# Kernel tuning notes

Hardware: AMD Instinct MI355X
Metric: run time of the kernel (lower is better)

Reference implementation:

```python
import jax, jax.numpy as jnp
import numpy as np

B, N, NT, ET = 16, 38, 9, 4
NE = N * (N - 1) // 2          # 703 edge-generation steps
R = N + NE                     # repeat_num = 741 masked subgraphs
H = D = 128                    # nhid / nout
L = 12                         # num_flow_layer
EDIM = ET - 1                  # 3 relation types used by RGCN
EPS = 1e-5
TEMP = 0.1                     # straight-through argmax temperature


def _st_dis(x, w1, b1, w2, b2):
    # MLP -> logits -> straight-through one-hot(argmax)
    h = jnp.tanh(x @ w1.T + b1)
    logits = h @ w2.T + b2
    soft = jax.nn.softmax(logits / TEMP, axis=-1)
    hard = jax.nn.one_hot(jnp.argmax(logits, axis=-1), logits.shape[-1], dtype=logits.dtype)
    return soft + jax.lax.stop_gradient(hard - soft)


def _one_hot_add(inputs, shift):
    # (inputs + shift) mod vocab in one-hot space == circular conv via FFT
    out = jnp.fft.ifft(jnp.fft.fft(inputs, axis=-1) * jnp.fft.fft(shift, axis=-1), axis=-1)
    return jnp.real(out).astype(inputs.dtype)


def _gconv(x, adj, w):
    # x: (b, n, f_in), adj: (b, e, n, n), w: (e*f_out, f_in)
    b, n, _ = x.shape
    s = (x @ w.T).reshape(b, n, EDIM, -1)            # (b, n, e, f_out)
    return jnp.einsum('beij,bjeo->bio', adj, s)      # aggregate over relations


def _rgcn(x, adj, emb_w, gc1_w, gc2_w, gc3_w):
    h = x @ emb_w.T
    h = jax.nn.relu(_gconv(h, adj, gc1_w))
    h = jax.nn.relu(_gconv(h, adj, gc2_w))
    return _gconv(h, adj, gc3_w)                     # no relu on last layer


def setup_inputs():
    key = jax.random.key(0)
    ks = jax.random.split(key, 16)
    s = 0.1
    iu, ju = np.triu_indices(N, k=1)                 # canonical edge order (703, 2)
    return {
        'x': jax.random.uniform(ks[0], (B, N, NT), dtype=jnp.float32),
        'adj': jax.random.uniform(ks[1], (B, ET, N, N), dtype=jnp.float32),
        'x_deq': jax.random.normal(ks[2], (B, N, NT), dtype=jnp.float32),
        'adj_deq': jax.random.normal(ks[3], (B, NE, ET), dtype=jnp.float32),
        'mask_node': jax.random.uniform(ks[4], (R, N)) < 0.5,
        'mask_edge': jax.random.uniform(ks[5], (R, N, N)) < 0.5,
        'index_select_edge': jnp.asarray(np.stack([iu, ju], 1), dtype=jnp.int32),
        'emb_w': jax.random.normal(ks[6], (NT, NT), jnp.float32) * s,
        'gc1_w': jax.random.normal(ks[7], (EDIM * H, NT), jnp.float32) * s,
        'gc2_w': jax.random.normal(ks[8], (EDIM * H, H), jnp.float32) * s,
        'gc3_w': jax.random.normal(ks[9], (EDIM * D, H), jnp.float32) * s,
        'bn_gamma': jnp.ones((D,), jnp.float32),
        'bn_beta': jnp.zeros((D,), jnp.float32),
        'node_w1': jax.random.normal(ks[10], (L, H, D), jnp.float32) * s,
        'node_b1': jnp.zeros((L, H), jnp.float32),
        'node_w2': jax.random.normal(ks[11], (L, NT, H), jnp.float32) * s,
        'node_b2': jnp.zeros((L, NT), jnp.float32),
        'edge_w1': jax.random.normal(ks[12], (L, H, 3 * D), jnp.float32) * s,
        'edge_b1': jnp.zeros((L, H), jnp.float32),
        'edge_w2': jax.random.normal(ks[13], (L, ET, H), jnp.float32) * s,
        'edge_b2': jnp.zeros((L, ET), jnp.float32),
    }


def reference(x, adj, x_deq, adj_deq, mask_node, mask_edge, index_select_edge,
              emb_w, gc1_w, gc2_w, gc3_w, bn_gamma, bn_beta,
              node_w1, node_b1, node_w2, node_b2,
              edge_w1, edge_b1, edge_w2, edge_b2):
    adj3 = adj[:, :EDIM]                                              # (B,3,N,N)
    xr = jnp.where(mask_node[None, :, :, None], x[:, None], 0.0)      # (B,R,N,NT)
    ar = jnp.where(mask_edge[None, :, None], adj3[:, None], 0.0)      # (B,R,3,N,N)
    xr = xr.reshape(B * R, N, NT)
    ar = ar.reshape(B * R, EDIM, N, N)
    node_emb = _rgcn(xr, ar, emb_w, gc1_w, gc2_w, gc3_w)              # (B*R,N,D)
    # BatchNorm1d over channels (training-mode batch statistics, biased var)
    m = node_emb.mean(axis=(0, 1))
    v = node_emb.var(axis=(0, 1))
    node_emb = (node_emb - m) * jax.lax.rsqrt(v + EPS) * bn_gamma + bn_beta
    node_emb = node_emb.reshape(B, R, N, D)
    graph_emb = node_emb.sum(axis=2)                                  # (B,R,D)
    graph_emb_node = graph_emb[:, :N]                                 # (B,N,D)
    graph_emb_edge = graph_emb[:, N:, None]                           # (B,NE,1,D)
    all_node_emb_edge = node_emb[:, N:]                               # (B,NE,N,D)
    idx = jnp.broadcast_to(index_select_edge[None, :, :, None].astype(jnp.int32), (B, NE, 2, D))
    sel = jnp.take_along_axis(all_node_emb_edge, idx, axis=2)         # (B,NE,2,D)
    graph_node_emb_edge = jnp.concatenate([sel, graph_emb_edge], axis=2).reshape(B, NE, 3 * D)
    xd, ad = x_deq, adj_deq
    for i in range(L):
        nt = _st_dis(graph_emb_node, node_w1[i], node_b1[i], node_w2[i], node_b2[i]).astype(x.dtype)
        xd = _one_hot_add(xd, nt)
        et = _st_dis(graph_node_emb_edge, edge_w1[i], edge_b1[i], edge_w2[i], edge_b2[i]).astype(adj.dtype)
        ad = _one_hot_add(ad, et)
    return (xd, ad)
```

## Files before the change

### kernel.cpp

```cpp
#include <hip/hip_runtime.h>

#define B_   16
#define N_   38
#define NT_  9
#define ET_  4
#define NE_  703
#define R_   741
#define L_   12
#define BR_  11856

__global__ __launch_bounds__(128) void k_sx(const float* __restrict__ x,
                                            const float* __restrict__ emb_w,
                                            const float* __restrict__ gc1_w,
                                            float* __restrict__ sx)
{
  int bn = blockIdx.x;
  int t  = threadIdx.x;
  __shared__ float xr[NT_];
  __shared__ float hx[NT_];
  if (t < NT_) xr[t] = x[bn*NT_ + t];
  __syncthreads();
  if (t < NT_) {
    float s = 0.f;
    #pragma unroll
    for (int u = 0; u < NT_; ++u) s += xr[u] * emb_w[t*NT_ + u];
    hx[t] = s;
  }
  __syncthreads();
  for (int eo = t; eo < 384; eo += 128) {
    float s = 0.f;
    #pragma unroll
    for (int u = 0; u < NT_; ++u) s += hx[u] * gc1_w[eo*NT_ + u];
    sx[bn*384 + eo] = s;
  }
}

__global__ __launch_bounds__(128) void k_wt(const float* __restrict__ gc2_w,
                                            const float* __restrict__ gc3_w,
                                            float* __restrict__ Wt)
{
  int blk   = blockIdx.x;
  int which = blk / 384;
  int rem   = blk - which*384;
  int e     = rem >> 7;
  int k     = rem & 127;
  int o     = threadIdx.x;
  const float* src = which ? gc3_w : gc2_w;
  Wt[(((which*3 + e) << 7) + k)*128 + o] = src[((e << 7) + o)*128 + k];
}

__device__ __forceinline__ void fma4(float4& d, float a, const float4& s) {
  d.x += a*s.x; d.y += a*s.y; d.z += a*s.z; d.w += a*s.w;
}

__device__ __forceinline__ void fill_A(const float* __restrict__ adj,
                                       const int* __restrict__ mask_edge,
                                       int b, int r, int e, int tid,
                                       float* __restrict__ A4_l,
                                       float* __restrict__ A1_l)
{
  for (int m = tid; m < 38*32; m += 256) {
    int j    = m >> 5;
    int slot = m & 31;
    int i    = (slot >> 2) + ((slot & 3) << 3);
    float v  = 0.f;
    if (mask_edge[(r*N_ + i)*N_ + j]) v = adj[((b*ET_ + e)*N_ + i)*N_ + j];
    A4_l[m] = v;
  }
  for (int m = tid; m < 38*8; m += 256) {
    int j = m >> 3;
    int i = (m & 7) + 32;
    float v = 0.f;
    if (i < N_ && mask_edge[(r*N_ + i)*N_ + j]) v = adj[((b*ET_ + e)*N_ + i)*N_ + j];
    A1_l[m] = v;
  }
}

__device__ __forceinline__ void eacc_m(const float* __restrict__ A4_l,
                                       const float* __restrict__ A1_l,
                                       const float* __restrict__ S_l,
                                       int p, int c,
                                       const int* __restrict__ mn,
                                       float4 d[5])
{
  #pragma unroll 2
  for (int j = 0; j < 38; ++j) {
    if (!mn[j]) continue;
    float4 s4 = *(const float4*)&S_l[(j << 7) + (c << 2)];
    float4 a4 = *(const float4*)&A4_l[(j << 5) + (p << 2)];
    float  a1 = A1_l[(j << 3) + p];
    fma4(d[0], a4.x, s4); fma4(d[1], a4.y, s4); fma4(d[2], a4.z, s4);
    fma4(d[3], a4.w, s4); fma4(d[4], a1,   s4);
  }
}

__device__ __forceinline__ void eacc_u(const float* __restrict__ A4_l,
                                       const float* __restrict__ A1_l,
                                       const float* __restrict__ S_l,
                                       int p, int c,
                                       float4 d[5])
{
  #pragma unroll 4
  for (int j = 0; j < 38; ++j) {
    float4 s4 = *(const float4*)&S_l[(j << 7) + (c << 2)];
    float4 a4 = *(const float4*)&A4_l[(j << 5) + (p << 2)];
    float  a1 = A1_l[(j << 3) + p];
    fma4(d[0], a4.x, s4); fma4(d[1], a4.y, s4); fma4(d[2], a4.z, s4);
    fma4(d[3], a4.w, s4); fma4(d[4], a1,   s4);
  }
}

__device__ __forceinline__ void gemm_fused(const float* __restrict__ H_l,
                                           const float* __restrict__ Wb,
                                           int p, int c, float4 g[3][5])
{
  #pragma unroll
  for (int e = 0; e < 3; ++e)
    #pragma unroll
    for (int q = 0; q < 5; ++q) { g[e][q].x = 0.f; g[e][q].y = 0.f; g[e][q].z = 0.f; g[e][q].w = 0.f; }
  #pragma unroll 1
  for (int k0 = 0; k0 < 128; k0 += 4) {
    float4 h0 = *(const float4*)&H_l[((p+ 0) << 7) + k0];
    float4 h1 = *(const float4*)&H_l[((p+ 8) << 7) + k0];
    float4 h2 = *(const float4*)&H_l[((p+16) << 7) + k0];
    float4 h3 = *(const float4*)&H_l[((p+24) << 7) + k0];
    float4 h4 = *(const float4*)&H_l[((p+32) << 7) + k0];
    #pragma unroll
    for (int e = 0; e < 3; ++e) {
      const float* We = &Wb[(e << 14) + (k0 << 7) + (c << 2)];
      float4 w0 = *(const float4*)&We[  0];
      float4 w1 = *(const float4*)&We[128];
      float4 w2 = *(const float4*)&We[256];
      float4 w3 = *(const float4*)&We[384];
      fma4(g[e][0], h0.x, w0); fma4(g[e][0], h0.y, w1); fma4(g[e][0], h0.z, w2); fma4(g[e][0], h0.w, w3);
      fma4(g[e][1], h1.x, w0); fma4(g[e][1], h1.y, w1); fma4(g[e][1], h1.z, w2); fma4(g[e][1], h1.w, w3);
      fma4(g[e][2], h2.x, w0); fma4(g[e][2], h2.y, w1); fma4(g[e][2], h2.z, w2); fma4(g[e][2], h2.w, w3);
      fma4(g[e][3], h3.x, w0); fma4(g[e][3], h3.y, w1); fma4(g[e][3], h3.z, w2); fma4(g[e][3], h3.w, w3);
      fma4(g[e][4], h4.x, w0); fma4(g[e][4], h4.y, w1); fma4(g[e][4], h4.z, w2); fma4(g[e][4], h4.w, w3);
    }
  }
}

__device__ __forceinline__ void relu_store(float* __restrict__ H_l, int p, int c,
                                           const float4 d[5])
{
  #pragma unroll
  for (int q = 0; q < 5; ++q) {
    float4 t;
    t.x = fmaxf(d[q].x, 0.f); t.y = fmaxf(d[q].y, 0.f);
    t.z = fmaxf(d[q].z, 0.f); t.w = fmaxf(d[q].w, 0.f);
    *(float4*)&H_l[((p + (q << 3)) << 7) + (c << 2)] = t;
  }
}

__global__ __launch_bounds__(256) void k_rgcn(
    const float* __restrict__ adj, const int* __restrict__ mask_node,
    const int* __restrict__ mask_edge, const int* __restrict__ isel,
    const float* __restrict__ sx, const float* __restrict__ Wt,
    float* __restrict__ sumE, float* __restrict__ sumSq,
    float* __restrict__ selw)
{
  const int br  = blockIdx.x;
  const int b   = br / R_;
  const int r   = br - b*R_;
  const int tid = threadIdx.x;
  const int c   = tid & 31;
  const int p   = tid >> 5;

  __shared__ __align__(16) float A4_l[38*32];
  __shared__ __align__(16) float A1_l[38*8];
  __shared__ __align__(16) float SH_l[40*128];
  __shared__ int mn_l[40];

  if (tid < 40) mn_l[tid] = (tid < 38) ? mask_node[r*N_ + tid] : 0;
  __syncthreads();

  float4 d[5];
  #pragma unroll
  for (int q = 0; q < 5; ++q) { d[q].x = d[q].y = d[q].z = d[q].w = 0.f; }

  for (int e = 0; e < 3; ++e) {
    for (int idx = tid; idx < 40*32; idx += 256) {
      int j = idx >> 5, q4 = idx & 31;
      float4 v; v.x = v.y = v.z = v.w = 0.f;
      if (j < N_ && mn_l[j]) v = *(const float4*)&sx[(b*N_ + j)*384 + (e << 7) + (q4 << 2)];
      *(float4*)&SH_l[(j << 7) + (q4 << 2)] = v;
    }
    fill_A(adj, mask_edge, b, r, e, tid, A4_l, A1_l);
    __syncthreads();
    eacc_m(A4_l, A1_l, SH_l, p, c, mn_l, d);
    __syncthreads();
  }
  relu_store(SH_l, p, c, d);
  __syncthreads();

  for (int gv = 0; gv < 2; ++gv) {
    float4 g[3][5];
    gemm_fused(SH_l, &Wt[gv*49152], p, c, g);
    #pragma unroll
    for (int q = 0; q < 5; ++q) { d[q].x = d[q].y = d[q].z = d[q].w = 0.f; }
    #pragma unroll
    for (int e = 0; e < 3; ++e) {
      __syncthreads();
      #pragma unroll
      for (int q = 0; q < 5; ++q)
        *(float4*)&SH_l[((p + (q << 3)) << 7) + (c << 2)] = g[e][q];
      fill_A(adj, mask_edge, b, r, e, tid, A4_l, A1_l);
      __syncthreads();
      eacc_u(A4_l, A1_l, SH_l, p, c, d);
    }
    if (gv == 0) {
      __syncthreads();
      relu_store(SH_l, p, c, d);
      __syncthreads();
    }
  }
  __syncthreads();

  {
    float4 sA, sB;
    sA.x = d[0].x+d[1].x+d[2].x+d[3].x+d[4].x;
    sA.y = d[0].y+d[1].y+d[2].y+d[3].y+d[4].y;
    sA.z = d[0].z+d[1].z+d[2].z+d[3].z+d[4].z;
    sA.w = d[0].w+d[1].w+d[2].w+d[3].w+d[4].w;
    sB.x = d[0].x*d[0].x+d[1].x*d[1].x+d[2].x*d[2].x+d[3].x*d[3].x+d[4].x*d[4].x;
    sB.y = d[0].y*d[0].y+d[1].y*d[1].y+d[2].y*d[2].y+d[3].y*d[3].y+d[4].y*d[4].y;
    sB.z = d[0].z*d[0].z+d[1].z*d[1].z+d[2].z*d[2].z+d[3].z*d[3].z+d[4].z*d[4].z;
    sB.w = d[0].w*d[0].w+d[1].w*d[1].w+d[2].w*d[2].w+d[3].w*d[3].w+d[4].w*d[4].w;
    *(float4*)&SH_l[( p      << 7) + (c << 2)] = sA;
    *(float4*)&SH_l[((8 + p) << 7) + (c << 2)] = sB;
  }
  __syncthreads();
  {
    int o = tid & 127, half = tid >> 7;
    float t = 0.f;
    #pragma unroll
    for (int pp = 0; pp < 8; ++pp) t += SH_l[(((half << 3) + pp) << 7) + o];
    if (half == 0) sumE [br*128 + o] = t;
    else           sumSq[br*128 + o] = t;
  }
  if (r >= N_) {
    int k  = r - N_;
    int iu = isel[2*k], ju = isel[2*k+1];
    if (p == (iu & 7)) {
      int mu = iu >> 3;
      float4 v = d[0];
      if (mu == 1) v = d[1]; else if (mu == 2) v = d[2];
      else if (mu == 3) v = d[3]; else if (mu == 4) v = d[4];
      *(float4*)&selw[(((b*NE_ + k)*2 + 0) << 7) + (c << 2)] = v;
    }
    if (p == (ju & 7)) {
      int mu = ju >> 3;
      float4 v = d[0];
      if (mu == 1) v = d[1]; else if (mu == 2) v = d[2];
      else if (mu == 3) v = d[3]; else if (mu == 4) v = d[4];
      *(float4*)&selw[(((b*NE_ + k)*2 + 1) << 7) + (c << 2)] = v;
    }
  }
}

__global__ __launch_bounds__(256) void k_bn1(const float* __restrict__ sumE,
                                             const float* __restrict__ sumSq,
                                             double* __restrict__ part)
{
  int g = blockIdx.x;
  int t = threadIdx.x;
  int o = t & 127, h = t >> 7;
  int lo = g*47;
  int hi = lo + 47; if (hi > BR_) hi = BR_;
  double a1 = 0.0, a2 = 0.0;
  for (int i = lo + h; i < hi; i += 2) {
    a1 += (double)sumE [i*128 + o];
    a2 += (double)sumSq[i*128 + o];
  }
  __shared__ double sh1[256], sh2[256];
  sh1[t] = a1; sh2[t] = a2;
  __syncthreads();
  if (h == 0) {
    part[g*128 + o]           = sh1[o] + sh1[128 + o];
    part[256*128 + g*128 + o] = sh2[o] + sh2[128 + o];
  }
}

__global__ __launch_bounds__(128) void k_bn2(const double* __restrict__ part,
                                             const float* __restrict__ gamma,
                                             const float* __restrict__ beta,
                                             float* __restrict__ bnsc,
                                             float* __restrict__ bnsh)
{
  int o = threadIdx.x;
  double s1 = 0.0, s2 = 0.0;
  for (int g = 0; g < 256; ++g) {
    s1 += part[g*128 + o];
    s2 += part[256*128 + g*128 + o];
  }
  double cnt = (double)BR_ * 38.0;
  double m   = s1 / cnt;
  double var = s2 / cnt - m*m;
  double rs  = 1.0 / sqrt(var + 1e-5);
  double sc  = (double)gamma[o] * rs;
  bnsc[o] = (float)sc;
  bnsh[o] = beta[o] - (float)(m * sc);
}

__global__ __launch_bounds__(128) void k_node(
    const float* __restrict__ sumE, const float* __restrict__ bnsc,
    const float* __restrict__ bnsh,
    const float* __restrict__ w1, const float* __restrict__ b1,
    const float* __restrict__ w2, const float* __restrict__ b2,
    const float* __restrict__ x_deq, float* __restrict__ out)
{
  int blk = blockIdx.x;
  int b   = blk / N_;
  int o   = threadIdx.x;
  __shared__ __align__(16) float xv[128];
  __shared__ __align__(16) float hb[128];
  __shared__ float lg[NT_];
  __shared__ int   P_s;
  int br = b*R_ + (blk - b*N_);
  xv[o] = sumE[br*128 + o]*bnsc[o] + 38.f*bnsh[o];
  if (o == 0) P_s = 0;
  __syncthreads();
  for (int l = 0; l < L_; ++l) {
    const float* wr = &w1[(l*128 + o)*128];
    float s = b1[l*128 + o];
    for (int k = 0; k < 128; k += 4) {
      float4 w4 = *(const float4*)&wr[k];
      s += w4.x*xv[k] + w4.y*xv[k+1] + w4.z*xv[k+2] + w4.w*xv[k+3];
    }
    hb[o] = tanhf(s);
    __syncthreads();
    if (o < NT_) {
      const float* w2r = &w2[(l*NT_ + o)*128];
      float s2 = b2[l*NT_ + o];
      for (int k = 0; k < 128; ++k) s2 += w2r[k]*hb[k];
      lg[o] = s2;
    }
    __syncthreads();
    if (o == 0) {
      int best = 0; float bv = lg[0];
      #pragma unroll
      for (int cc = 1; cc < NT_; ++cc) if (lg[cc] > bv) { bv = lg[cc]; best = cc; }
      P_s += best;
    }
    __syncthreads();
  }
  int P = P_s % NT_;
  if (o < NT_) {
    int srcc = o - P; if (srcc < 0) srcc += NT_;
    out[blk*NT_ + o] = x_deq[blk*NT_ + srcc];
  }
}

__global__ __launch_bounds__(256) void k_edge(
    const float* __restrict__ sumE, const float* __restrict__ selw,
    const float* __restrict__ bnsc, const float* __restrict__ bnsh,
    const float* __restrict__ w1, const float* __restrict__ b1,
    const float* __restrict__ w2, const float* __restrict__ b2,
    const float* __restrict__ adj_deq, float* __restrict__ out)
{
  int k = blockIdx.x;
  int t = threadIdx.x;
  int o = t & 127, g = t >> 7;
  __shared__ __align__(16) float xv[16][384];
  __shared__ __align__(16) float hb[16][132];
  __shared__ float lg[16][4];
  __shared__ int   Pf[16];

  for (int idx = t; idx < 16*128; idx += 256) {
    int b = idx >> 7, oo = idx & 127;
    float sc = bnsc[oo], sh = bnsh[oo];
    int base = ((b*NE_ + k)*2)*128;
    xv[b][oo]       = selw[base + oo]      *sc + sh;
    xv[b][128 + oo] = selw[base + 128 + oo]*sc + sh;
    xv[b][256 + oo] = sumE[(b*R_ + N_ + k)*128 + oo]*sc + 38.f*sh;
  }
  int Preg = 0;
  __syncthreads();

  for (int l = 0; l < L_; ++l) {
    float acc[8];
    #pragma unroll
    for (int bb = 0; bb < 8; ++bb) acc[bb] = b1[l*128 + o];
    const float* wr = &w1[(l*128 + o)*384];
    for (int kk = 0; kk < 384; kk += 4) {
      float4 w4 = *(const float4*)&wr[kk];
      #pragma unroll
      for (int bb = 0; bb < 8; ++bb) {
        float4 h4 = *(const float4*)&xv[g*8 + bb][kk];
        acc[bb] += w4.x*h4.x + w4.y*h4.y + w4.z*h4.z + w4.w*h4.w;
      }
    }
    #pragma unroll
    for (int bb = 0; bb < 8; ++bb) hb[g*8 + bb][o] = tanhf(acc[bb]);
    __syncthreads();
    if (t < 64) {
      int m = t >> 2, c = t & 3;
      const float* w2r = &w2[(l*ET_ + c)*128];
      float s2 = b2[l*ET_ + c];
      for (int kk = 0; kk < 128; ++kk) s2 += w2r[kk]*hb[m][kk];
      lg[m][c] = s2;
    }
    __syncthreads();
    if (t < 16) {
      int best = 0; float bv = lg[t][0];
      #pragma unroll
      for (int c = 1; c < ET_; ++c) if (lg[t][c] > bv) { bv = lg[t][c]; best = c; }
      Preg += best;
    }
    __syncthreads();
  }
  if (t < 16) Pf[t] = Preg & 3;
  __syncthreads();
  if (t < 64) {
    int m = t >> 2, c = t & 3;
    int srcc = c - Pf[m]; if (srcc < 0) srcc += ET_;
    out[(m*NE_ + k)*ET_ + c] = adj_deq[(m*NE_ + k)*ET_ + srcc];
  }
}

extern "C" void kernel_launch(void* const* d_in, const int* in_sizes, int n_in,
                              void* d_out, int out_size, void* d_ws, size_t ws_size,
                              hipStream_t stream)
{
  (void)in_sizes; (void)n_in; (void)out_size; (void)ws_size;

  const float* x         = (const float*)d_in[0];
  const float* adj       = (const float*)d_in[1];
  const float* x_deq     = (const float*)d_in[2];
  const float* adj_deq   = (const float*)d_in[3];
  const int*   mask_node = (const int*)d_in[4];
  const int*   mask_edge = (const int*)d_in[5];
  const int*   isel      = (const int*)d_in[6];
  const float* emb_w     = (const float*)d_in[7];
  const float* gc1_w     = (const float*)d_in[8];
  const float* gc2_w     = (const float*)d_in[9];
  const float* gc3_w     = (const float*)d_in[10];
  const float* bn_gamma  = (const float*)d_in[11];
  const float* bn_beta   = (const float*)d_in[12];
  const float* node_w1   = (const float*)d_in[13];
  const float* node_b1   = (const float*)d_in[14];
  const float* node_w2   = (const float*)d_in[15];
  const float* node_b2   = (const float*)d_in[16];
  const float* edge_w1   = (const float*)d_in[17];
  const float* edge_b1   = (const float*)d_in[18];
  const float* edge_w2   = (const float*)d_in[19];
  const float* edge_b2   = (const float*)d_in[20];

  float* out_f = (float*)d_out;

  float*  wsf   = (float*)d_ws;
  float*  sx    = wsf;
  float*  sumE  = sx    + 233472;
  float*  sumSq = sumE  + 1517568;
  float*  selw  = sumSq + 1517568;
  float*  bnsc  = selw  + 2879488;
  float*  bnsh  = bnsc  + 128;
  double* part  = (double*)(bnsh + 128);
  float*  Wt    = (float*)part;

  k_wt  <<<768,    128, 0, stream>>>(gc2_w, gc3_w, Wt);
  k_sx  <<<B_*N_,  128, 0, stream>>>(x, emb_w, gc1_w, sx);
  k_rgcn<<<BR_,    256, 0, stream>>>(adj, mask_node, mask_edge, isel, sx,
                                     Wt, sumE, sumSq, selw);
  k_bn1 <<<256,    256, 0, stream>>>(sumE, sumSq, part);
  k_bn2 <<<1,      128, 0, stream>>>(part, bn_gamma, bn_beta, bnsc, bnsh);
  k_node<<<B_*N_,  128, 0, stream>>>(sumE, bnsc, bnsh, node_w1, node_b1,
                                     node_w2, node_b2, x_deq, out_f);
  k_edge<<<NE_,    256, 0, stream>>>(sumE, selw, bnsc, bnsh, edge_w1, edge_b1,
                                     edge_w2, edge_b2, adj_deq,
                                     out_f + B_*N_*NT_);
}
```

Before: 2.496 ms.

## Cache all three masked adjacency slices in LDS and prefetch next slice

The masked adjacency for each relation is now loaded once into a three-slot shared-memory buffer and reused across all three RGCN layers, where before it was re-gathered from global memory nine times. The load for the next relation is issued into registers before the current aggregation runs, so global latency overlaps with compute. This raises shared memory per block by roughly 10 KB, which may reduce how many blocks fit on each CU.

```diff
diff --git a/kernel.cpp b/kernel.cpp
--- a/kernel.cpp
+++ b/kernel.cpp
@@ -53,31 +53,59 @@
   d.x += a*s.x; d.y += a*s.y; d.z += a*s.z; d.w += a*s.w;
 }
 
-__device__ __forceinline__ void fill_A(const float* __restrict__ adj,
-                                       const int* __restrict__ mask_edge,
-                                       int b, int r, int e, int tid,
-                                       float* __restrict__ A4_l,
-                                       float* __restrict__ A1_l)
-{
-  for (int m = tid; m < 38*32; m += 256) {
-    int j    = m >> 5;
-    int slot = m & 31;
-    int i    = (slot >> 2) + ((slot & 3) << 3);
-    float v  = 0.f;
-    if (mask_edge[(r*N_ + i)*N_ + j]) v = adj[((b*ET_ + e)*N_ + i)*N_ + j];
-    A4_l[m] = v;
-  }
-  for (int m = tid; m < 38*8; m += 256) {
-    int j = m >> 3;
-    int i = (m & 7) + 32;
+__device__ __forceinline__ void ldA(const float* __restrict__ adj,
+                                    const int* __restrict__ mask_edge,
+                                    int b, int r, int e, int tid,
+                                    float av[5], float a1v[2])
+{
+  #pragma unroll
+  for (int t = 0; t < 5; ++t) {
+    int m = tid + (t << 8);
     float v = 0.f;
-    if (i < N_ && mask_edge[(r*N_ + i)*N_ + j]) v = adj[((b*ET_ + e)*N_ + i)*N_ + j];
-    A1_l[m] = v;
-  }
-}
-
-__device__ __forceinline__ void eacc_m(const float* __restrict__ A4_l,
-                                       const float* __restrict__ A1_l,
+    if (m < 1216) {
+      int j = m >> 5, slot = m & 31;
+      int i = (slot >> 2) + ((slot & 3) << 3);
+      int   msk = mask_edge[(r*N_ + i)*N_ + j];
+      float a   = adj[((b*ET_ + e)*N_ + i)*N_ + j];
+      v = msk ? a : 0.f;
+    }
+    av[t] = v;
+  }
+  #pragma unroll
+  for (int t = 0; t < 2; ++t) {
+    int m = tid + (t << 8);
+    float v = 0.f;
+    if (m < 304) {
+      int j = m >> 3;
+      int i = (m & 7) + 32;
+      if (i < N_) {
+        int   msk = mask_edge[(r*N_ + i)*N_ + j];
+        float a   = adj[((b*ET_ + e)*N_ + i)*N_ + j];
+        v = msk ? a : 0.f;
+      }
+    }
+    a1v[t] = v;
+  }
+}
+
+__device__ __forceinline__ void stA(float* __restrict__ A4e,
+                                    float* __restrict__ A1e, int tid,
+                                    const float av[5], const float a1v[2])
+{
+  #pragma unroll
+  for (int t = 0; t < 5; ++t) {
+    int m = tid + (t << 8);
+    if (m < 1216) A4e[m] = av[t];
+  }
+  #pragma unroll
+  for (int t = 0; t < 2; ++t) {
+    int m = tid + (t << 8);
+    if (m < 304) A1e[m] = a1v[t];
+  }
+}
+
+__device__ __forceinline__ void eacc_m(const float* __restrict__ A4e,
+                                       const float* __restrict__ A1e,
                                        const float* __restrict__ S_l,
                                        int p, int c,
                                        const int* __restrict__ mn,
@@ -87,15 +115,15 @@
   for (int j = 0; j < 38; ++j) {
     if (!mn[j]) continue;
     float4 s4 = *(const float4*)&S_l[(j << 7) + (c << 2)];
-    float4 a4 = *(const float4*)&A4_l[(j << 5) + (p << 2)];
-    float  a1 = A1_l[(j << 3) + p];
+    float4 a4 = *(const float4*)&A4e[(j << 5) + (p << 2)];
+    float  a1 = A1e[(j << 3) + p];
     fma4(d[0], a4.x, s4); fma4(d[1], a4.y, s4); fma4(d[2], a4.z, s4);
     fma4(d[3], a4.w, s4); fma4(d[4], a1,   s4);
   }
 }
 
-__device__ __forceinline__ void eacc_u(const float* __restrict__ A4_l,
-                                       const float* __restrict__ A1_l,
+__device__ __forceinline__ void eacc_u(const float* __restrict__ A4e,
+                                       const float* __restrict__ A1e,
                                        const float* __restrict__ S_l,
                                        int p, int c,
                                        float4 d[5])
@@ -103,8 +131,8 @@
   #pragma unroll 4
   for (int j = 0; j < 38; ++j) {
     float4 s4 = *(const float4*)&S_l[(j << 7) + (c << 2)];
-    float4 a4 = *(const float4*)&A4_l[(j << 5) + (p << 2)];
-    float  a1 = A1_l[(j << 3) + p];
+    float4 a4 = *(const float4*)&A4e[(j << 5) + (p << 2)];
+    float  a1 = A1e[(j << 3) + p];
     fma4(d[0], a4.x, s4); fma4(d[1], a4.y, s4); fma4(d[2], a4.z, s4);
     fma4(d[3], a4.w, s4); fma4(d[4], a1,   s4);
   }
@@ -167,12 +195,15 @@
   const int c   = tid & 31;
   const int p   = tid >> 5;
 
-  __shared__ __align__(16) float A4_l[38*32];
-  __shared__ __align__(16) float A1_l[38*8];
+  __shared__ __align__(16) float A4_l[3*1216];
+  __shared__ __align__(16) float A1_l[3*304];
   __shared__ __align__(16) float SH_l[40*128];
   __shared__ int mn_l[40];
 
   if (tid < 40) mn_l[tid] = (tid < 38) ? mask_node[r*N_ + tid] : 0;
+
+  float av[5], a1v[2];
+  ldA(adj, mask_edge, b, r, 0, tid, av, a1v);
   __syncthreads();
 
   float4 d[5];
@@ -186,9 +217,10 @@
       if (j < N_ && mn_l[j]) v = *(const float4*)&sx[(b*N_ + j)*384 + (e << 7) + (q4 << 2)];
       *(float4*)&SH_l[(j << 7) + (q4 << 2)] = v;
     }
-    fill_A(adj, mask_edge, b, r, e, tid, A4_l, A1_l);
-    __syncthreads();
-    eacc_m(A4_l, A1_l, SH_l, p, c, mn_l, d);
+    stA(&A4_l[e*1216], &A1_l[e*304], tid, av, a1v);
+    __syncthreads();
+    if (e < 2) ldA(adj, mask_edge, b, r, e+1, tid, av, a1v);
+    eacc_m(&A4_l[e*1216], &A1_l[e*304], SH_l, p, c, mn_l, d);
     __syncthreads();
   }
   relu_store(SH_l, p, c, d);
@@ -205,9 +237,8 @@
       #pragma unroll
       for (int q = 0; q < 5; ++q)
         *(float4*)&SH_l[((p + (q << 3)) << 7) + (c << 2)] = g[e][q];
-      fill_A(adj, mask_edge, b, r, e, tid, A4_l, A1_l);
       __syncthreads();
-      eacc_u(A4_l, A1_l, SH_l, p, c, d);
+      eacc_u(&A4_l[e*1216], &A1_l[e*304], SH_l, p, c, d);
     }
     if (gv == 0) {
       __syncthreads();
```

New measurement: 2.242 ms. 1.11x faster.
